# Performance work log

Measured on AMD Instinct MI355X. Metric: run time of the kernel, lower is better.

Reference implementation:

```python
import jax, jax.numpy as jnp
import numpy as np

# dims
N, E, HID = 20000, 320000, 128
L, H = 12, 4            # num_layers, heads
C = 2 * HID             # h width = in_channels = out_channels*heads = 256
OC = C // H             # per-head out channels = 64
FF = 4 * HID            # ffn hidden = 512
LN_EPS = 1e-5
SLOPE = 0.2             # GATConv leaky_relu negative slope


def _layer_norm(x, g, b):
    m = x.mean(-1, keepdims=True)
    v = ((x - m) ** 2).mean(-1, keepdims=True)
    return (x - m) * jax.lax.rsqrt(v + LN_EPS) * g + b


def setup_inputs() -> dict:
    key = jax.random.key(0)
    ks = jax.random.split(key, 16)
    s = 0.05
    f32 = jnp.float32
    return {
        "hf": jax.random.normal(ks[0], (N, HID), f32),
        "hs": jax.random.normal(ks[1], (N, HID), f32),
        "edge_index": jax.random.randint(ks[2], (2, E), 0, N, dtype=jnp.int32),
        # GATConv params (stacked over layers)
        "W": jax.random.normal(ks[3], (L, C, H * OC), f32) * s,       # lin (no bias)
        "att_src": jax.random.normal(ks[4], (L, H, OC), f32) * s,
        "att_dst": jax.random.normal(ks[5], (L, H, OC), f32) * s,
        "gat_b": jax.random.normal(ks[6], (L, C), f32) * s,            # GATConv bias
        # FFN params
        "w1": jax.random.normal(ks[7], (L, C, FF), f32) * s,
        "b1": jax.random.normal(ks[8], (L, FF), f32) * s,
        "w2": jax.random.normal(ks[9], (L, FF, C), f32) * s,
        "b2": jax.random.normal(ks[10], (L, C), f32) * s,
        # LayerNorm params
        "ln1_g": jnp.ones((L, C), f32),
        "ln1_b": jnp.zeros((L, C), f32),
        "ln2_g": jnp.ones((L, C), f32),
        "ln2_b": jnp.zeros((L, C), f32),
    }


def reference(hf, hs, edge_index, W, att_src, att_dst, gat_b,
              w1, b1, w2, b2, ln1_g, ln1_b, ln2_g, ln2_b):
    # PyG GATConv add_self_loops=True
    loop = jnp.arange(N, dtype=edge_index.dtype)
    src = jnp.concatenate([edge_index[0], loop])  # [E+N]
    dst = jnp.concatenate([edge_index[1], loop])

    h = jnp.concatenate([hf, hs], axis=-1)  # [N, C]
    for i in range(L):
        # --- GATConv + residual + LN (dropout = identity at eval) ---
        r = h
        xh = (h @ W[i]).reshape(N, H, OC)              # [N,H,OC]
        a_s = (xh * att_src[i]).sum(-1)                # [N,H]
        a_d = (xh * att_dst[i]).sum(-1)                # [N,H]
        e = jax.nn.leaky_relu(a_s[src] + a_d[dst], SLOPE)          # [E+N,H]
        m = jax.ops.segment_max(e, dst, num_segments=N)            # [N,H]
        ex = jnp.exp(e - m[dst])
        z = jax.ops.segment_sum(ex, dst, num_segments=N)           # [N,H]
        alpha = ex / z[dst]                                        # segment softmax
        msg = xh[src] * alpha[..., None]                           # [E+N,H,OC]
        out = jax.ops.segment_sum(msg, dst, num_segments=N).reshape(N, C) + gat_b[i]
        h = _layer_norm(out + r, ln1_g[i], ln1_b[i])
        # --- FFN + residual + LN ---
        r = h
        f = jax.nn.relu(h @ w1[i] + b1[i]) @ w2[i] + b2[i]
        h = _layer_norm(f + r, ln2_g[i], ln2_b[i])

    return h[:, :HID], h[:, HID:]
```

## Files before the change

### kernel.cpp

```cpp
#include <hip/hip_runtime.h>
#include <hip/hip_bf16.h>
#include <math.h>

#define C_DIM 256
#define HID 128
#define HEADS 4
#define OC 64
#define FF_DIM 512
#define NLAYERS 12

constexpr float LN_EPS = 1e-5f;
constexpr float SLOPE  = 0.2f;

typedef __attribute__((ext_vector_type(4))) float f32x4;
typedef __attribute__((ext_vector_type(8))) short bf16x8_t;
typedef __attribute__((ext_vector_type(4))) int i32x4;

__device__ __forceinline__ float leaky(float x) { return x > 0.f ? x : SLOPE * x; }

__device__ __forceinline__ float bf2f(unsigned short u) {
    union { unsigned i; float f; } v; v.i = ((unsigned)u) << 16; return v.f;
}
__device__ __forceinline__ void bf2x(unsigned u, float& lo, float& hi) {
    union { unsigned i; float f; } a, b;
    a.i = u << 16; b.i = u & 0xffff0000u;
    lo = a.f; hi = b.f;
}
__device__ __forceinline__ unsigned packbf(float lo, float hi) {
    unsigned a = __bfloat16_as_ushort(__float2bfloat16(lo));
    unsigned b = __bfloat16_as_ushort(__float2bfloat16(hi));
    return a | (b << 16);
}

__global__ void zero_i32_kernel(int* __restrict__ p, int n) {
    int i = blockIdx.x * blockDim.x + threadIdx.x;
    if (i < n) p[i] = 0;
}

__global__ void concat_kernel(const float* __restrict__ hf, const float* __restrict__ hs,
                              float* __restrict__ h, __hip_bfloat16* __restrict__ hb, int Nn) {
    int idx = blockIdx.x * blockDim.x + threadIdx.x;
    int total = Nn * C_DIM;
    if (idx < total) {
        int n = idx >> 8;
        int c = idx & 255;
        float v = (c < HID) ? hf[n * HID + c] : hs[n * HID + (c - HID)];
        h[idx] = v;
        hb[idx] = __float2bfloat16(v);
    }
}

__global__ void transp_bf16_kernel(const float* __restrict__ in,
                                   __hip_bfloat16* __restrict__ out, int K, int N) {
    __shared__ float t[32][33];
    const float* inl = in + (size_t)blockIdx.z * K * N;
    __hip_bfloat16* outl = out + (size_t)blockIdx.z * K * N;
    int kb = blockIdx.y * 32, nb = blockIdx.x * 32;
    int tx = threadIdx.x & 31, ty = threadIdx.x >> 5;
    #pragma unroll
    for (int r = 0; r < 32; r += 8)
        t[ty + r][tx] = inl[(size_t)(kb + ty + r) * N + nb + tx];
    __syncthreads();
    #pragma unroll
    for (int r = 0; r < 32; r += 8)
        outl[(size_t)(nb + ty + r) * K + kb + tx] = __float2bfloat16(t[tx][ty + r]);
}

__global__ void hist_kernel(const int* __restrict__ dst, int* __restrict__ counts, int E) {
    int e = blockIdx.x * blockDim.x + threadIdx.x;
    if (e < E) atomicAdd(&counts[dst[e]], 1);
}

__global__ void scan_kernel(const int* __restrict__ counts, int* __restrict__ offsets,
                            int* __restrict__ cursor, int n) {
    __shared__ int wsum[16];
    __shared__ int carry_s;
    const int lane = threadIdx.x & 63, wid = threadIdx.x >> 6;
    if (threadIdx.x == 0) carry_s = 0;
    __syncthreads();
    for (int base = 0; base < n; base += 1024) {
        int i = base + (int)threadIdx.x;
        int v = (i < n) ? counts[i] : 0;
        int x = v;
        #pragma unroll
        for (int off = 1; off < 64; off <<= 1) {
            int t = __shfl_up(x, off);
            if (lane >= off) x += t;
        }
        if (lane == 63) wsum[wid] = x;
        __syncthreads();
        if (threadIdx.x == 0) {
            int acc = carry_s;
            #pragma unroll
            for (int w = 0; w < 16; ++w) { int t = wsum[w]; wsum[w] = acc; acc += t; }
            carry_s = acc;
        }
        __syncthreads();
        int excl = wsum[wid] + x - v;
        if (i < n) { offsets[i] = excl; cursor[i] = excl; }
        __syncthreads();
    }
    if (threadIdx.x == 0) offsets[n] = carry_s;
}

__global__ void fill_kernel(const int* __restrict__ src, const int* __restrict__ dst,
                            int* __restrict__ cursor, int* __restrict__ csr_src, int E) {
    int e = blockIdx.x * blockDim.x + threadIdx.x;
    if (e < E) {
        int d = dst[e];
        int p = atomicAdd(&cursor[d], 1);
        csr_src[p] = src[e];
    }
}

#define GBM 64
#define GBN 64
#define GBK 64
#define GLS 72

__global__ __launch_bounds__(256) void gemm_bf16_kernel(
    const __hip_bfloat16* __restrict__ A,
    const __hip_bfloat16* __restrict__ BT,
    const float* __restrict__ bias,
    __hip_bfloat16* __restrict__ Cb,
    const float* __restrict__ attS,
    const float* __restrict__ attD,
    float* __restrict__ aS,
    float* __restrict__ aD,
    int M, int N, int K, int relu)
{
    __shared__ short As[GBM * GLS];
    __shared__ short Bs[GBN * GLS];
    __shared__ float attP[2][2][GBM];
    const int tid = threadIdx.x;
    const int wave = tid >> 6, lane = tid & 63;
    const int lr = lane & 15, lq = lane >> 4;
    const int wm = (wave >> 1) * 32, wn = (wave & 1) * 32;
    const int row0 = blockIdx.x * GBM, col0 = blockIdx.y * GBN;

    const int sr = tid >> 2;
    const int sc = (tid & 3) * 16;

    f32x4 acc[2][2] = {};

    for (int k0 = 0; k0 < K; k0 += GBK) {
        int gr = row0 + sr;
        i32x4 va0 = {}, va1 = {};
        if (gr < M) {
            const __hip_bfloat16* ap = &A[(size_t)gr * K + k0 + sc];
            va0 = *(const i32x4*)ap;
            va1 = *(const i32x4*)(ap + 8);
        }
        *(i32x4*)&As[sr * GLS + sc] = va0;
        *(i32x4*)&As[sr * GLS + sc + 8] = va1;
        const __hip_bfloat16* bp = &BT[(size_t)(col0 + sr) * K + k0 + sc];
        *(i32x4*)&Bs[sr * GLS + sc] = *(const i32x4*)bp;
        *(i32x4*)&Bs[sr * GLS + sc + 8] = *(const i32x4*)(bp + 8);
        __syncthreads();

        #pragma unroll
        for (int ks = 0; ks < 2; ++ks) {
            bf16x8_t af[2], bfr[2];
            #pragma unroll
            for (int t = 0; t < 2; ++t) {
                af[t]  = *(const bf16x8_t*)&As[(wm + t * 16 + lr) * GLS + ks * 32 + lq * 8];
                bfr[t] = *(const bf16x8_t*)&Bs[(wn + t * 16 + lr) * GLS + ks * 32 + lq * 8];
            }
            #pragma unroll
            for (int mt = 0; mt < 2; ++mt)
                #pragma unroll
                for (int nt = 0; nt < 2; ++nt)
                    acc[mt][nt] = __builtin_amdgcn_mfma_f32_16x16x32_bf16(
                        af[mt], bfr[nt], acc[mt][nt], 0, 0, 0);
        }
        __syncthreads();
    }

    float bv[2];
    #pragma unroll
    for (int nt = 0; nt < 2; ++nt)
        bv[nt] = bias ? bias[col0 + wn + nt * 16 + lr] : 0.f;

    #pragma unroll
    for (int mt = 0; mt < 2; ++mt) {
        #pragma unroll
        for (int r = 0; r < 4; ++r) {
            int grow = row0 + wm + mt * 16 + lq * 4 + r;
            if (grow >= M) continue;
            #pragma unroll
            for (int nt = 0; nt < 2; ++nt) {
                float v = acc[mt][nt][r] + bv[nt];
                if (relu) v = fmaxf(v, 0.f);
                Cb[(size_t)grow * N + col0 + wn + nt * 16 + lr] = __float2bfloat16(v);
            }
        }
    }

    if (aS) {
        const int head = col0 >> 6;
        float atS[2], atD[2];
        #pragma unroll
        for (int nt = 0; nt < 2; ++nt) {
            int c = col0 + wn + nt * 16 + lr;
            atS[nt] = attS[c];
            atD[nt] = attD[c];
        }
        #pragma unroll
        for (int mt = 0; mt < 2; ++mt) {
            #pragma unroll
            for (int r = 0; r < 4; ++r) {
                float vs = acc[mt][0][r] * atS[0] + acc[mt][1][r] * atS[1];
                float vd = acc[mt][0][r] * atD[0] + acc[mt][1][r] * atD[1];
                #pragma unroll
                for (int off = 1; off < 16; off <<= 1) {
                    vs += __shfl_xor(vs, off);
                    vd += __shfl_xor(vd, off);
                }
                if (lr == 0) {
                    int rl = wm + mt * 16 + lq * 4 + r;
                    attP[wave & 1][0][rl] = vs;
                    attP[wave & 1][1][rl] = vd;
                }
            }
        }
        __syncthreads();
        if (tid < GBM) {
            int grow = row0 + tid;
            if (grow < M) {
                aS[grow * HEADS + head] = attP[0][0][tid] + attP[1][0][tid];
                aD[grow * HEADS + head] = attP[0][1][tid] + attP[1][1][tid];
            }
        }
    }
}

__global__ __launch_bounds__(256) void agg_kernel(
    const __hip_bfloat16* __restrict__ xhb, const float* __restrict__ a_s,
    const float* __restrict__ a_d, const int* __restrict__ csr,
    const int* __restrict__ offs, const float* __restrict__ gat_b,
    const float* __restrict__ ln_g, const float* __restrict__ ln_b,
    float* __restrict__ h, __hip_bfloat16* __restrict__ hb, int Nn)
{
    const int lane = threadIdx.x & 63;
    const int n = __builtin_amdgcn_readfirstlane(blockIdx.x * 4 + (threadIdx.x >> 6));
    if (n >= Nn) return;
    const int half = lane >> 5;
    const int sl = lane & 31;
    const int head = sl >> 3;
    const int c0 = sl * 8;
    const unsigned* x = (const unsigned*)xhb;
    const size_t rowp = (size_t)n * (C_DIM / 2) + (c0 >> 1);

    const float ad = a_d[n * 4 + head];

    const int beg = offs[n], end = offs[n + 1];
    const int ne = end - beg;
    const int nh0 = (ne + 1) >> 1;
    int ih  = half ? (beg + nh0) : beg;
    int cnt = half ? (ne - nh0) : nh0;

    float acc[8] = {};
    float z = 0.f;

    {
        float wself = __expf(leaky(a_s[n * 4 + head] + ad));
        if (half) {
            i32x4 xv = *(const i32x4*)&x[rowp];
            #pragma unroll
            for (int q = 0; q < 4; ++q) {
                float lo, hi; bf2x((unsigned)xv[q], lo, hi);
                acc[2 * q]     = wself * lo;
                acc[2 * q + 1] = wself * hi;
            }
            z = wself;
        }
    }

    for (; cnt >= 4; cnt -= 4, ih += 4) {
        int s0 = csr[ih], s1 = csr[ih + 1], s2 = csr[ih + 2], s3 = csr[ih + 3];
        float w0 = __expf(leaky(a_s[s0 * 4 + head] + ad));
        float w1 = __expf(leaky(a_s[s1 * 4 + head] + ad));
        float w2 = __expf(leaky(a_s[s2 * 4 + head] + ad));
        float w3 = __expf(leaky(a_s[s3 * 4 + head] + ad));
        i32x4 x0 = *(const i32x4*)&x[(size_t)s0 * (C_DIM / 2) + (c0 >> 1)];
        i32x4 x1 = *(const i32x4*)&x[(size_t)s1 * (C_DIM / 2) + (c0 >> 1)];
        i32x4 x2 = *(const i32x4*)&x[(size_t)s2 * (C_DIM / 2) + (c0 >> 1)];
        i32x4 x3 = *(const i32x4*)&x[(size_t)s3 * (C_DIM / 2) + (c0 >> 1)];
        #pragma unroll
        for (int q = 0; q < 4; ++q) {
            float lo, hi;
            bf2x((unsigned)x0[q], lo, hi);
            acc[2 * q] += w0 * lo; acc[2 * q + 1] += w0 * hi;
            bf2x((unsigned)x1[q], lo, hi);
            acc[2 * q] += w1 * lo; acc[2 * q + 1] += w1 * hi;
            bf2x((unsigned)x2[q], lo, hi);
            acc[2 * q] += w2 * lo; acc[2 * q + 1] += w2 * hi;
            bf2x((unsigned)x3[q], lo, hi);
            acc[2 * q] += w3 * lo; acc[2 * q + 1] += w3 * hi;
        }
        z += (w0 + w1) + (w2 + w3);
    }
    for (; cnt > 0; --cnt, ++ih) {
        int s0 = csr[ih];
        float w0 = __expf(leaky(a_s[s0 * 4 + head] + ad));
        i32x4 x0 = *(const i32x4*)&x[(size_t)s0 * (C_DIM / 2) + (c0 >> 1)];
        #pragma unroll
        for (int q = 0; q < 4; ++q) {
            float lo, hi; bf2x((unsigned)x0[q], lo, hi);
            acc[2 * q] += w0 * lo; acc[2 * q + 1] += w0 * hi;
        }
        z += w0;
    }

    #pragma unroll
    for (int j = 0; j < 8; ++j) acc[j] += __shfl_xor(acc[j], 32);
    z += __shfl_xor(z, 32);

    float4 res0 = *(const float4*)&h[(size_t)n * C_DIM + c0];
    float4 res1 = *(const float4*)&h[(size_t)n * C_DIM + c0 + 4];
    float4 gb0 = *(const float4*)&gat_b[c0];
    float4 gb1 = *(const float4*)&gat_b[c0 + 4];
    float rz = 1.0f / z;
    float val[8];
    val[0] = acc[0] * rz + gb0.x + res0.x;
    val[1] = acc[1] * rz + gb0.y + res0.y;
    val[2] = acc[2] * rz + gb0.z + res0.z;
    val[3] = acc[3] * rz + gb0.w + res0.w;
    val[4] = acc[4] * rz + gb1.x + res1.x;
    val[5] = acc[5] * rz + gb1.y + res1.y;
    val[6] = acc[6] * rz + gb1.z + res1.z;
    val[7] = acc[7] * rz + gb1.w + res1.w;

    float s1 = 0.f, s2 = 0.f;
    #pragma unroll
    for (int j = 0; j < 8; ++j) { s1 += val[j]; s2 += val[j] * val[j]; }
    #pragma unroll
    for (int off = 1; off < 64; off <<= 1) {
        s1 += __shfl_xor(s1, off);
        s2 += __shfl_xor(s2, off);
    }
    float mean = s1 * (1.0f / (2 * C_DIM));
    float inv = rsqrtf(s2 * (1.0f / (2 * C_DIM)) - mean * mean + LN_EPS);

    if (half == 0) {
        float4 g0 = *(const float4*)&ln_g[c0];
        float4 g1 = *(const float4*)&ln_g[c0 + 4];
        float4 bb0 = *(const float4*)&ln_b[c0];
        float4 bb1 = *(const float4*)&ln_b[c0 + 4];
        float o[8];
        o[0] = (val[0] - mean) * inv * g0.x + bb0.x;
        o[1] = (val[1] - mean) * inv * g0.y + bb0.y;
        o[2] = (val[2] - mean) * inv * g0.z + bb0.z;
        o[3] = (val[3] - mean) * inv * g0.w + bb0.w;
        o[4] = (val[4] - mean) * inv * g1.x + bb1.x;
        o[5] = (val[5] - mean) * inv * g1.y + bb1.y;
        o[6] = (val[6] - mean) * inv * g1.z + bb1.z;
        o[7] = (val[7] - mean) * inv * g1.w + bb1.w;
        float4 o0 = {o[0], o[1], o[2], o[3]};
        float4 o1 = {o[4], o[5], o[6], o[7]};
        *(float4*)&h[(size_t)n * C_DIM + c0] = o0;
        *(float4*)&h[(size_t)n * C_DIM + c0 + 4] = o1;
        i32x4 ob;
        ob[0] = (int)packbf(o[0], o[1]);
        ob[1] = (int)packbf(o[2], o[3]);
        ob[2] = (int)packbf(o[4], o[5]);
        ob[3] = (int)packbf(o[6], o[7]);
        *(i32x4*)&((unsigned*)hb)[rowp] = ob;
    }
}

__global__ __launch_bounds__(256) void ln2_kernel(
    const __hip_bfloat16* __restrict__ fb, const float* __restrict__ ln_g,
    const float* __restrict__ ln_b, float* __restrict__ h,
    __hip_bfloat16* __restrict__ hb, float* __restrict__ out_split, int Nn)
{
    const int lane = threadIdx.x & 63;
    const int n = __builtin_amdgcn_readfirstlane(blockIdx.x * 4 + (threadIdx.x >> 6));
    if (n >= Nn) return;
    const int c0 = lane * 4;
    const unsigned short* f = (const unsigned short*)fb;

    float4 res = *(const float4*)&h[(size_t)n * C_DIM + c0];
    ushort4 fv = *(const ushort4*)&f[(size_t)n * C_DIM + c0];
    float val[4];
    val[0] = bf2f(fv.x) + res.x;
    val[1] = bf2f(fv.y) + res.y;
    val[2] = bf2f(fv.z) + res.z;
    val[3] = bf2f(fv.w) + res.w;

    float s1 = (val[0] + val[1]) + (val[2] + val[3]);
    float s2 = (val[0] * val[0] + val[1] * val[1]) + (val[2] * val[2] + val[3] * val[3]);
    #pragma unroll
    for (int off = 1; off < 64; off <<= 1) {
        s1 += __shfl_xor(s1, off);
        s2 += __shfl_xor(s2, off);
    }
    float mean = s1 * (1.0f / C_DIM);
    float inv = rsqrtf(s2 * (1.0f / C_DIM) - mean * mean + LN_EPS);
    float4 g = *(const float4*)&ln_g[c0];
    float4 bb = *(const float4*)&ln_b[c0];
    float4 o;
    o.x = (val[0] - mean) * inv * g.x + bb.x;
    o.y = (val[1] - mean) * inv * g.y + bb.y;
    o.z = (val[2] - mean) * inv * g.z + bb.z;
    o.w = (val[3] - mean) * inv * g.w + bb.w;

    if (out_split) {
        size_t off_ = (c0 < HID) ? ((size_t)n * HID + c0)
                                 : ((size_t)Nn * HID + (size_t)n * HID + (c0 - HID));
        *(float4*)&out_split[off_] = o;
    } else {
        *(float4*)&h[(size_t)n * C_DIM + c0] = o;
        ushort4 ob;
        ob.x = __bfloat16_as_ushort(__float2bfloat16(o.x));
        ob.y = __bfloat16_as_ushort(__float2bfloat16(o.y));
        ob.z = __bfloat16_as_ushort(__float2bfloat16(o.z));
        ob.w = __bfloat16_as_ushort(__float2bfloat16(o.w));
        *(ushort4*)&((unsigned short*)hb)[(size_t)n * C_DIM + c0] = ob;
    }
}

extern "C" void kernel_launch(void* const* d_in, const int* in_sizes, int n_in,
                              void* d_out, int out_size, void* d_ws, size_t ws_size,
                              hipStream_t stream)
{
    const float* hf       = (const float*)d_in[0];
    const float* hs       = (const float*)d_in[1];
    const int*   edge     = (const int*)  d_in[2];
    const float* W        = (const float*)d_in[3];
    const float* att_src  = (const float*)d_in[4];
    const float* att_dst  = (const float*)d_in[5];
    const float* gat_b    = (const float*)d_in[6];
    const float* w1       = (const float*)d_in[7];
    const float* b1       = (const float*)d_in[8];
    const float* w2       = (const float*)d_in[9];
    const float* b2       = (const float*)d_in[10];
    const float* ln1g     = (const float*)d_in[11];
    const float* ln1b     = (const float*)d_in[12];
    const float* ln2g     = (const float*)d_in[13];
    const float* ln2b     = (const float*)d_in[14];
    float* out = (float*)d_out;

    const int N = in_sizes[0] / HID;
    const int E = in_sizes[2] / 2;
    const int* e_src = edge;
    const int* e_dst = edge + E;

    char* p = (char*)d_ws;
    auto alloc = [&](size_t bytes) {
        char* r = p;
        p += (bytes + 255) & ~(size_t)255;
        return (void*)r;
    };
    float*          h      = (float*)alloc((size_t)N * C_DIM * 4);
    __hip_bfloat16* hb     = (__hip_bfloat16*)alloc((size_t)N * C_DIM * 2);
    __hip_bfloat16* xhb    = (__hip_bfloat16*)alloc((size_t)N * C_DIM * 2);
    __hip_bfloat16* fbuf   = (__hip_bfloat16*)alloc((size_t)N * C_DIM * 2);
    __hip_bfloat16* midb   = (__hip_bfloat16*)alloc((size_t)N * FF_DIM * 2);
    float*          a_s    = (float*)alloc((size_t)N * HEADS * 4);
    float*          a_d    = (float*)alloc((size_t)N * HEADS * 4);
    int*            counts = (int*)alloc((size_t)N * 4);
    int*            offs   = (int*)alloc((size_t)(N + 1) * 4);
    int*            cursor = (int*)alloc((size_t)N * 4);
    int*            csr    = (int*)alloc((size_t)E * 4);
    __hip_bfloat16* WT     = (__hip_bfloat16*)alloc((size_t)NLAYERS * C_DIM * C_DIM * 2);
    __hip_bfloat16* w1T    = (__hip_bfloat16*)alloc((size_t)NLAYERS * C_DIM * FF_DIM * 2);
    __hip_bfloat16* w2T    = (__hip_bfloat16*)alloc((size_t)NLAYERS * FF_DIM * C_DIM * 2);

    {
        int total = N * C_DIM;
        concat_kernel<<<(total + 255) / 256, 256, 0, stream>>>(hf, hs, h, hb, N);
    }
    transp_bf16_kernel<<<dim3(C_DIM / 32, C_DIM / 32, NLAYERS), 256, 0, stream>>>(W, WT, C_DIM, C_DIM);
    transp_bf16_kernel<<<dim3(FF_DIM / 32, C_DIM / 32, NLAYERS), 256, 0, stream>>>(w1, w1T, C_DIM, FF_DIM);
    transp_bf16_kernel<<<dim3(C_DIM / 32, FF_DIM / 32, NLAYERS), 256, 0, stream>>>(w2, w2T, FF_DIM, C_DIM);

    zero_i32_kernel<<<(N + 255) / 256, 256, 0, stream>>>(counts, N);
    hist_kernel<<<(E + 255) / 256, 256, 0, stream>>>(e_dst, counts, E);
    scan_kernel<<<1, 1024, 0, stream>>>(counts, offs, cursor, N);
    fill_kernel<<<(E + 255) / 256, 256, 0, stream>>>(e_src, e_dst, cursor, csr, E);

    const int gm = (N + GBM - 1) / GBM;

    for (int l = 0; l < NLAYERS; ++l) {
        const __hip_bfloat16* Wl  = WT  + (size_t)l * C_DIM * C_DIM;
        const __hip_bfloat16* w1l = w1T + (size_t)l * C_DIM * FF_DIM;
        const __hip_bfloat16* w2l = w2T + (size_t)l * FF_DIM * C_DIM;
        const float* asl  = att_src + (size_t)l * C_DIM;
        const float* adl  = att_dst + (size_t)l * C_DIM;
        const float* gbl  = gat_b + (size_t)l * C_DIM;
        const float* b1l  = b1 + (size_t)l * FF_DIM;
        const float* b2l  = b2 + (size_t)l * C_DIM;
        const float* g1l  = ln1g + (size_t)l * C_DIM;
        const float* be1l = ln1b + (size_t)l * C_DIM;
        const float* g2l  = ln2g + (size_t)l * C_DIM;
        const float* be2l = ln2b + (size_t)l * C_DIM;

        gemm_bf16_kernel<<<dim3(gm, C_DIM / GBN), 256, 0, stream>>>(
            hb, Wl, nullptr, xhb, asl, adl, a_s, a_d, N, C_DIM, C_DIM, 0);
        agg_kernel<<<(N + 3) / 4, 256, 0, stream>>>(
            xhb, a_s, a_d, csr, offs, gbl, g1l, be1l, h, hb, N);
        gemm_bf16_kernel<<<dim3(gm, FF_DIM / GBN), 256, 0, stream>>>(
            hb, w1l, b1l, midb, nullptr, nullptr, nullptr, nullptr,
            N, FF_DIM, C_DIM, 1);
        gemm_bf16_kernel<<<dim3(gm, C_DIM / GBN), 256, 0, stream>>>(
            midb, w2l, b2l, fbuf, nullptr, nullptr, nullptr, nullptr,
            N, C_DIM, FF_DIM, 0);
        ln2_kernel<<<(N + 3) / 4, 256, 0, stream>>>(
            fbuf, g2l, be2l, h, hb, (l == NLAYERS - 1) ? out : nullptr, N);
    }
}
```

Baseline: 1.264 ms.

## Fuse FFN GEMMs, bias/ReLU, residual and LayerNorm into one kernel

Replaces the two FFN GEMM launches and the separate LN2 kernel with a single kernel per 32-row tile. The ReLU intermediate stays in shared memory and the second GEMM output feeds straight into residual add and LayerNorm, so the N×512 and N×256 bf16 buffers never make a round trip through global memory. In exchange, weight B-fragments are read directly from global memory with no LDS staging. The small 32-row tile also means each block re-reads the full w1/w2, and the in-place hb read/write relies on each block only touching its own rows.

```diff
diff --git a/kernel.cpp b/kernel.cpp
--- a/kernel.cpp
+++ b/kernel.cpp
@@ -369,55 +369,137 @@
     }
 }
 
-__global__ __launch_bounds__(256) void ln2_kernel(
-    const __hip_bfloat16* __restrict__ fb, const float* __restrict__ ln_g,
-    const float* __restrict__ ln_b, float* __restrict__ h,
-    __hip_bfloat16* __restrict__ hb, float* __restrict__ out_split, int Nn)
+#define FBM 32
+#define FPAD 264
+#define MPAD 520
+
+__global__ __launch_bounds__(256) void ffn_kernel(
+    const __hip_bfloat16* __restrict__ hbin,
+    const __hip_bfloat16* __restrict__ w1T,
+    const float* __restrict__ b1,
+    const __hip_bfloat16* __restrict__ w2T,
+    const float* __restrict__ b2,
+    const float* __restrict__ ln_g, const float* __restrict__ ln_b,
+    float* __restrict__ h, __hip_bfloat16* __restrict__ hbout,
+    float* __restrict__ out_split, int Nn)
 {
-    const int lane = threadIdx.x & 63;
-    const int n = __builtin_amdgcn_readfirstlane(blockIdx.x * 4 + (threadIdx.x >> 6));
-    if (n >= Nn) return;
-    const int c0 = lane * 4;
-    const unsigned short* f = (const unsigned short*)fb;
-
-    float4 res = *(const float4*)&h[(size_t)n * C_DIM + c0];
-    ushort4 fv = *(const ushort4*)&f[(size_t)n * C_DIM + c0];
-    float val[4];
-    val[0] = bf2f(fv.x) + res.x;
-    val[1] = bf2f(fv.y) + res.y;
-    val[2] = bf2f(fv.z) + res.z;
-    val[3] = bf2f(fv.w) + res.w;
-
-    float s1 = (val[0] + val[1]) + (val[2] + val[3]);
-    float s2 = (val[0] * val[0] + val[1] * val[1]) + (val[2] * val[2] + val[3] * val[3]);
-    #pragma unroll
-    for (int off = 1; off < 64; off <<= 1) {
-        s1 += __shfl_xor(s1, off);
-        s2 += __shfl_xor(s2, off);
-    }
-    float mean = s1 * (1.0f / C_DIM);
-    float inv = rsqrtf(s2 * (1.0f / C_DIM) - mean * mean + LN_EPS);
-    float4 g = *(const float4*)&ln_g[c0];
-    float4 bb = *(const float4*)&ln_b[c0];
-    float4 o;
-    o.x = (val[0] - mean) * inv * g.x + bb.x;
-    o.y = (val[1] - mean) * inv * g.y + bb.y;
-    o.z = (val[2] - mean) * inv * g.z + bb.z;
-    o.w = (val[3] - mean) * inv * g.w + bb.w;
-
-    if (out_split) {
-        size_t off_ = (c0 < HID) ? ((size_t)n * HID + c0)
-                                 : ((size_t)Nn * HID + (size_t)n * HID + (c0 - HID));
-        *(float4*)&out_split[off_] = o;
-    } else {
-        *(float4*)&h[(size_t)n * C_DIM + c0] = o;
-        ushort4 ob;
-        ob.x = __bfloat16_as_ushort(__float2bfloat16(o.x));
-        ob.y = __bfloat16_as_ushort(__float2bfloat16(o.y));
-        ob.z = __bfloat16_as_ushort(__float2bfloat16(o.z));
-        ob.w = __bfloat16_as_ushort(__float2bfloat16(o.w));
-        *(ushort4*)&((unsigned short*)hb)[(size_t)n * C_DIM + c0] = ob;
-    }
+    __shared__ short Ah[FBM * FPAD];
+    __shared__ short Mid[FBM * MPAD];
+    __shared__ float Red[4][FBM][2];
+    const int tid = threadIdx.x;
+    const int wave = tid >> 6, lane = tid & 63;
+    const int lr = lane & 15, lq = lane >> 4;
+    const int row0 = blockIdx.x * FBM;
+
+    #pragma unroll
+    for (int c = 0; c < 4; ++c) {
+        int chunk = tid + c * 256;
+        int r = chunk >> 5, col = (chunk & 31) * 8;
+        i32x4 v = *(const i32x4*)&hbin[(size_t)(row0 + r) * C_DIM + col];
+        *(i32x4*)&Ah[r * FPAD + col] = v;
+    }
+    __syncthreads();
+
+    const int fcol0 = wave * 128;
+    f32x4 acc1[2][8] = {};
+    for (int k0 = 0; k0 < C_DIM; k0 += 32) {
+        bf16x8_t af0 = *(const bf16x8_t*)&Ah[(lr) * FPAD + k0 + lq * 8];
+        bf16x8_t af1 = *(const bf16x8_t*)&Ah[(16 + lr) * FPAD + k0 + lq * 8];
+        #pragma unroll
+        for (int nt = 0; nt < 8; ++nt) {
+            bf16x8_t bf = *(const bf16x8_t*)&w1T[(size_t)(fcol0 + nt * 16 + lr) * C_DIM + k0 + lq * 8];
+            acc1[0][nt] = __builtin_amdgcn_mfma_f32_16x16x32_bf16(af0, bf, acc1[0][nt], 0, 0, 0);
+            acc1[1][nt] = __builtin_amdgcn_mfma_f32_16x16x32_bf16(af1, bf, acc1[1][nt], 0, 0, 0);
+        }
+    }
+    #pragma unroll
+    for (int nt = 0; nt < 8; ++nt) {
+        float bv = b1[fcol0 + nt * 16 + lr];
+        #pragma unroll
+        for (int mt = 0; mt < 2; ++mt)
+            #pragma unroll
+            for (int r = 0; r < 4; ++r) {
+                float v = fmaxf(acc1[mt][nt][r] + bv, 0.f);
+                Mid[(mt * 16 + lq * 4 + r) * MPAD + fcol0 + nt * 16 + lr] =
+                    (short)__bfloat16_as_ushort(__float2bfloat16(v));
+            }
+    }
+    __syncthreads();
+
+    const int ccol0 = wave * 64;
+    f32x4 acc2[2][4] = {};
+    for (int k0 = 0; k0 < FF_DIM; k0 += 32) {
+        bf16x8_t af0 = *(const bf16x8_t*)&Mid[(lr) * MPAD + k0 + lq * 8];
+        bf16x8_t af1 = *(const bf16x8_t*)&Mid[(16 + lr) * MPAD + k0 + lq * 8];
+        #pragma unroll
+        for (int nt = 0; nt < 4; ++nt) {
+            bf16x8_t bf = *(const bf16x8_t*)&w2T[(size_t)(ccol0 + nt * 16 + lr) * FF_DIM + k0 + lq * 8];
+            acc2[0][nt] = __builtin_amdgcn_mfma_f32_16x16x32_bf16(af0, bf, acc2[0][nt], 0, 0, 0);
+            acc2[1][nt] = __builtin_amdgcn_mfma_f32_16x16x32_bf16(af1, bf, acc2[1][nt], 0, 0, 0);
+        }
+    }
+
+    float b2v[4];
+    #pragma unroll
+    for (int nt = 0; nt < 4; ++nt) b2v[nt] = b2[ccol0 + nt * 16 + lr];
+
+    float vals[2][4][4];
+    #pragma unroll
+    for (int mt = 0; mt < 2; ++mt)
+        #pragma unroll
+        for (int r = 0; r < 4; ++r) {
+            int rowg = row0 + mt * 16 + lq * 4 + r;
+            float ps1 = 0.f, ps2 = 0.f;
+            #pragma unroll
+            for (int nt = 0; nt < 4; ++nt) {
+                float v = acc2[mt][nt][r] + b2v[nt] +
+                          h[(size_t)rowg * C_DIM + ccol0 + nt * 16 + lr];
+                vals[mt][nt][r] = v;
+                ps1 += v;
+                ps2 += v * v;
+            }
+            #pragma unroll
+            for (int off = 1; off < 16; off <<= 1) {
+                ps1 += __shfl_xor(ps1, off);
+                ps2 += __shfl_xor(ps2, off);
+            }
+            if (lr == 0) {
+                Red[wave][mt * 16 + lq * 4 + r][0] = ps1;
+                Red[wave][mt * 16 + lq * 4 + r][1] = ps2;
+            }
+        }
+    __syncthreads();
+
+    float gv[4], bbv[4];
+    #pragma unroll
+    for (int nt = 0; nt < 4; ++nt) {
+        gv[nt]  = ln_g[ccol0 + nt * 16 + lr];
+        bbv[nt] = ln_b[ccol0 + nt * 16 + lr];
+    }
+    #pragma unroll
+    for (int mt = 0; mt < 2; ++mt)
+        #pragma unroll
+        for (int r = 0; r < 4; ++r) {
+            int rl = mt * 16 + lq * 4 + r;
+            int rowg = row0 + rl;
+            float s1 = Red[0][rl][0] + Red[1][rl][0] + Red[2][rl][0] + Red[3][rl][0];
+            float s2 = Red[0][rl][1] + Red[1][rl][1] + Red[2][rl][1] + Red[3][rl][1];
+            float mean = s1 * (1.0f / C_DIM);
+            float inv = rsqrtf(s2 * (1.0f / C_DIM) - mean * mean + LN_EPS);
+            #pragma unroll
+            for (int nt = 0; nt < 4; ++nt) {
+                int col = ccol0 + nt * 16 + lr;
+                float o = (vals[mt][nt][r] - mean) * inv * gv[nt] + bbv[nt];
+                if (out_split) {
+                    size_t off_ = (col < HID) ? ((size_t)rowg * HID + col)
+                                              : ((size_t)Nn * HID + (size_t)rowg * HID + (col - HID));
+                    out_split[off_] = o;
+                } else {
+                    h[(size_t)rowg * C_DIM + col] = o;
+                    hbout[(size_t)rowg * C_DIM + col] = __float2bfloat16(o);
+                }
+            }
+        }
 }
 
 extern "C" void kernel_launch(void* const* d_in, const int* in_sizes, int n_in,
@@ -455,8 +537,6 @@
     float*          h      = (float*)alloc((size_t)N * C_DIM * 4);
     __hip_bfloat16* hb     = (__hip_bfloat16*)alloc((size_t)N * C_DIM * 2);
     __hip_bfloat16* xhb    = (__hip_bfloat16*)alloc((size_t)N * C_DIM * 2);
-    __hip_bfloat16* fbuf   = (__hip_bfloat16*)alloc((size_t)N * C_DIM * 2);
-    __hip_bfloat16* midb   = (__hip_bfloat16*)alloc((size_t)N * FF_DIM * 2);
     float*          a_s    = (float*)alloc((size_t)N * HEADS * 4);
     float*          a_d    = (float*)alloc((size_t)N * HEADS * 4);
     int*            counts = (int*)alloc((size_t)N * 4);
@@ -481,6 +561,7 @@
     fill_kernel<<<(E + 255) / 256, 256, 0, stream>>>(e_src, e_dst, cursor, csr, E);
 
     const int gm = (N + GBM - 1) / GBM;
+    const int fm = N / FBM;
 
     for (int l = 0; l < NLAYERS; ++l) {
         const __hip_bfloat16* Wl  = WT  + (size_t)l * C_DIM * C_DIM;
@@ -500,13 +581,8 @@
             hb, Wl, nullptr, xhb, asl, adl, a_s, a_d, N, C_DIM, C_DIM, 0);
         agg_kernel<<<(N + 3) / 4, 256, 0, stream>>>(
             xhb, a_s, a_d, csr, offs, gbl, g1l, be1l, h, hb, N);
-        gemm_bf16_kernel<<<dim3(gm, FF_DIM / GBN), 256, 0, stream>>>(
-            hb, w1l, b1l, midb, nullptr, nullptr, nullptr, nullptr,
-            N, FF_DIM, C_DIM, 1);
-        gemm_bf16_kernel<<<dim3(gm, C_DIM / GBN), 256, 0, stream>>>(
-            midb, w2l, b2l, fbuf, nullptr, nullptr, nullptr, nullptr,
-            N, C_DIM, FF_DIM, 0);
-        ln2_kernel<<<(N + 3) / 4, 256, 0, stream>>>(
-            fbuf, g2l, be2l, h, hb, (l == NLAYERS - 1) ? out : nullptr, N);
-    }
-}
+        ffn_kernel<<<fm, 256, 0, stream>>>(
+            hb, w1l, b1l, w2l, b2l, g2l, be2l, h, hb,
+            (l == NLAYERS - 1) ? out : nullptr, N);
+    }
+}
```

Result: slower. 1.667 ms (+31.8%).
